# Performance work log

Hardware: AMD Instinct MI355X
Metric: run time of the kernel (lower is better)

Reference implementation:

```python
import jax, jax.numpy as jnp
import numpy as np

L = 64        # label_size = len(label2id)
START = 62    # label2id['START']
STOP = 63     # label2id['STOP']
T = 200000    # sequence length
NEG = -10000.0


def setup_inputs() -> dict:
    key = jax.random.key(0)
    k1, k2 = jax.random.split(key)
    lstm_feats = jax.random.normal(k1, (1, T, L), dtype=jnp.float32)
    transitions = jax.random.normal(k2, (L, L), dtype=jnp.float32)
    # CRF constructor masks: cannot transition INTO START, cannot transition FROM STOP
    transitions = transitions.at[START, :].set(NEG).at[:, STOP].set(NEG)
    return {"lstm_feats": lstm_feats, "transitions": transitions}


def reference(lstm_feats, transitions):
    # Viterbi decode, vectorized over tags; lax.scan over time replaces the
    # nested Python loops of the original (same recurrence, same math).
    feats = lstm_feats[0]  # (T, L)
    init = jnp.full((L,), NEG, dtype=lstm_feats.dtype).at[START].set(0.0)

    def step(v, feat):
        # scores[next, prev] = v[prev] + transitions[next, prev]
        scores = v[None, :] + transitions          # (L, L)
        bp = jnp.argmax(scores, axis=1).astype(jnp.int32)  # backpointers per next_tag
        v_new = jnp.max(scores, axis=1) + feat     # viterbi vars + emission
        return v_new, bp

    v, bptrs = jax.lax.scan(step, init, feats)     # bptrs: (T, L)

    terminal = v + transitions[STOP]               # (L,)
    best = jnp.argmax(terminal).astype(jnp.int32)
    path_score = terminal[best]

    # Backtrack: reverse scan emits the tag chosen at each time step, in order.
    def back(tag, bp):
        return bp[tag], tag

    _, best_path = jax.lax.scan(back, best, bptrs, reverse=True)  # (T,) int32
    return path_score, best_path
```

## Files before the change

kernel.cpp:

```cpp
#include <hip/hip_runtime.h>

#define L 64
#define TLEN 200000
#define CH 528
#define NCH 379
#define LASTLEN (TLEN - (NCH - 1) * CH)
#define NEGV -10000.0f
#define STARTT 62
#define STOPT 63

#define CKPT_OFF 0
#define M_OFF ((NCH + 1) * L * 4)
#define ETAG_OFF (M_OFF + NCH * L)

typedef float f32x4 __attribute__((ext_vector_type(4)));

#define WAVE_BARRIER() __asm__ volatile("s_waitcnt lgkmcnt(0)\ns_barrier" ::: "memory")
#define FAST_BARRIER() __asm__ volatile("s_barrier" ::: "memory")
#define STEP_BARRIER() __asm__ volatile("" ::: "memory")

__device__ __forceinline__ float max3f(float a, float b, float c) {
    float r;
    __asm__("v_max3_f32 %0, %1, %2, %3" : "=v"(r) : "v"(a), "v"(b), "v"(c));
    return r;
}

#define QPERM(x, ctrl)                                                         \
    __int_as_float(__builtin_amdgcn_update_dpp(                                \
        __float_as_int(x), __float_as_int(x), ctrl, 0xf, 0xf, false))

__global__ __launch_bounds__(256, 1) void k_forward(const float* __restrict__ feats,
                                                    const float* __restrict__ trans,
                                                    float* __restrict__ ckpt) {
    const int tid = threadIdx.x;
    const int l = tid & 63;
    const int w = tid >> 6;
    const int d = 16 * w + (l >> 2);
    const int g = l & 3;
    const bool writer = (g == 0);

    const f32x4* t4 = reinterpret_cast<const f32x4*>(trans) + d * 16 + g * 4;
    f32x4 q0 = t4[0], q1 = t4[1], q2 = t4[2], q3 = t4[3];
    __asm__ volatile("" : "+v"(q0), "+v"(q1), "+v"(q2), "+v"(q3));

    __shared__ __align__(16) float vbuf[2][L];

    float vq = (d == STARTT) ? 0.0f : NEGV;
    if (writer) vbuf[0][d] = vq;
    WAVE_BARRIER();

    float fc[8];
#pragma unroll
    for (int j = 0; j < 8; ++j) fc[j] = feats[j * L + d];

    int nextck = 0, cidx = 0;

#define FWD_STEP(RD, WR, FEAT)                                                 \
    do {                                                                       \
        const f32x4 va0 = *reinterpret_cast<const f32x4*>(&vbuf[RD][16 * g + 0]);  \
        const f32x4 va1 = *reinterpret_cast<const f32x4*>(&vbuf[RD][16 * g + 4]);  \
        const f32x4 va2 = *reinterpret_cast<const f32x4*>(&vbuf[RD][16 * g + 8]);  \
        const f32x4 va3 = *reinterpret_cast<const f32x4*>(&vbuf[RD][16 * g + 12]); \
        const f32x4 s0 = va0 + q0, s1 = va1 + q1, s2 = va2 + q2, s3 = va3 + q3;    \
        const float m0 = max3f(fmaxf(s0.x, s0.y), s0.z, s0.w);                 \
        const float m1 = max3f(fmaxf(s1.x, s1.y), s1.z, s1.w);                 \
        const float m2 = max3f(fmaxf(s2.x, s2.y), s2.z, s2.w);                 \
        const float m3 = max3f(fmaxf(s3.x, s3.y), s3.z, s3.w);                 \
        float x = fmaxf(max3f(m0, m1, m2), m3);                                \
        x = fmaxf(x, QPERM(x, 0xB1));                                          \
        x = fmaxf(x, QPERM(x, 0x4E));                                          \
        vq = x + (FEAT);                                                       \
        if (writer) vbuf[WR][d] = vq;                                          \
        FAST_BARRIER();                                                        \
    } while (0)

    for (int tb = 0; tb < TLEN; tb += 8) {
        if (tb == nextck) {
            if (writer) ckpt[cidx * L + d] = vq;
            nextck += CH;
            ++cidx;
        }
        float fn_[8];
        const bool more = (tb + 8) < TLEN;
        if (more) {
#pragma unroll
            for (int j = 0; j < 8; ++j) fn_[j] = feats[(tb + 8 + j) * L + d];
        }
        FWD_STEP(0, 1, fc[0]);
        FWD_STEP(1, 0, fc[1]);
        FWD_STEP(0, 1, fc[2]);
        FWD_STEP(1, 0, fc[3]);
        FWD_STEP(0, 1, fc[4]);
        FWD_STEP(1, 0, fc[5]);
        FWD_STEP(0, 1, fc[6]);
        FWD_STEP(1, 0, fc[7]);
        if (more) {
#pragma unroll
            for (int j = 0; j < 8; ++j) fc[j] = fn_[j];
        }
    }
    if (writer) ckpt[NCH * L + d] = vq;
#undef FWD_STEP
}

__device__ __forceinline__ void load_trow(const float* __restrict__ trans, int n, float* trow) {
#pragma unroll
    for (int i = 0; i < 16; ++i) {
        const f32x4 q = reinterpret_cast<const f32x4*>(trans)[n * 16 + i];
        trow[4 * i + 0] = q.x;
        trow[4 * i + 1] = q.y;
        trow[4 * i + 2] = q.z;
        trow[4 * i + 3] = q.w;
    }
}

__device__ __forceinline__ void replay_chunk(const float* __restrict__ feats,
                                             const float* __restrict__ ckpt,
                                             const float* trow, float* vsh,
                                             unsigned char* bpl, int c, int len, int n) {
    float vreg = ckpt[c * L + n];
    vsh[n] = vreg;
    STEP_BARRIER();
    const int base = c * CH;

    float fc[8];
#pragma unroll
    for (int j = 0; j < 8; ++j) fc[j] = feats[(base + j) * L + n];

    for (int sb = 0; sb < len; sb += 8) {
        float fn_[8];
        const bool more = (sb + 8) < len;
        if (more) {
#pragma unroll
            for (int j = 0; j < 8; ++j) fn_[j] = feats[(base + sb + 8 + j) * L + n];
        }
#pragma unroll
        for (int j = 0; j < 8; ++j) {
            float mc[4];
            int ic[4];
#pragma unroll
            for (int g = 0; g < 4; ++g) {
                float m = -INFINITY;
                int idx = g * 16;
#pragma unroll
                for (int r = 0; r < 4; ++r) {
                    const int pb = g * 16 + r * 4;
                    const f32x4 vv = *reinterpret_cast<const f32x4*>(vsh + pb);
                    const float a = vv.x + trow[pb + 0];
                    const float b = vv.y + trow[pb + 1];
                    const float cc = vv.z + trow[pb + 2];
                    const float d = vv.w + trow[pb + 3];
                    if (a > m)  { m = a;  idx = pb + 0; }
                    if (b > m)  { m = b;  idx = pb + 1; }
                    if (cc > m) { m = cc; idx = pb + 2; }
                    if (d > m)  { m = d;  idx = pb + 3; }
                }
                mc[g] = m;
                ic[g] = idx;
            }
            float m = mc[0];
            int idx = ic[0];
            if (mc[1] > m) { m = mc[1]; idx = ic[1]; }
            if (mc[2] > m) { m = mc[2]; idx = ic[2]; }
            if (mc[3] > m) { m = mc[3]; idx = ic[3]; }

            vreg = m + fc[j];
            bpl[(sb + j) * L + n] = (unsigned char)idx;
            vsh[n] = vreg;
            STEP_BARRIER();
        }
        if (more) {
#pragma unroll
            for (int j = 0; j < 8; ++j) fc[j] = fn_[j];
        }
    }
}

__global__ __launch_bounds__(64, 1) void k_maps(const float* __restrict__ feats,
                                                const float* __restrict__ trans,
                                                const float* __restrict__ ckpt,
                                                unsigned char* __restrict__ M) {
    const int c = blockIdx.x;
    const int n = threadIdx.x;
    const int len = (c == NCH - 1) ? LASTLEN : CH;

    __shared__ __align__(16) float vsh[L];
    __shared__ unsigned char bpl[CH * L];

    float trow[L];
    load_trow(trans, n, trow);
    replay_chunk(feats, ckpt, trow, vsh, bpl, c, len, n);
    __syncthreads();

    int tag = n;
    for (int s = len - 1; s >= 0; --s) tag = bpl[s * L + tag];
    M[c * L + n] = (unsigned char)tag;
}

__global__ __launch_bounds__(64, 1) void k_stitch(const float* __restrict__ trans,
                                                  const float* __restrict__ ckpt,
                                                  const unsigned char* __restrict__ M,
                                                  int* __restrict__ etag,
                                                  float* __restrict__ out) {
    const int n = threadIdx.x;
    __shared__ float tsh[L];
    __shared__ int bsh;
    __shared__ __align__(16) unsigned char msh[NCH * L];

    tsh[n] = ckpt[NCH * L + n] + trans[STOPT * L + n];
    __syncthreads();
    if (n == 0) {
        float m = tsh[0];
        int b = 0;
        for (int p = 1; p < L; ++p)
            if (tsh[p] > m) { m = tsh[p]; b = p; }
        out[0] = m;
        bsh = b;
    }
    __syncthreads();

    for (int i = n; i < (NCH * L) / 4; i += L)
        reinterpret_cast<int*>(msh)[i] = reinterpret_cast<const int*>(M)[i];
    __syncthreads();

    if (n == 0) {
        int carry = bsh;
        for (int c = NCH - 1; c >= 1; --c) {
            etag[c] = carry;
            carry = msh[c * L + carry];
        }
        etag[0] = carry;
    }
}

__global__ __launch_bounds__(64, 1) void k_emit(const float* __restrict__ feats,
                                                const float* __restrict__ trans,
                                                const float* __restrict__ ckpt,
                                                const int* __restrict__ etag,
                                                float* __restrict__ out) {
    const int c = blockIdx.x;
    const int n = threadIdx.x;
    const int len = (c == NCH - 1) ? LASTLEN : CH;

    __shared__ __align__(16) float vsh[L];
    __shared__ unsigned char bpl[CH * L];
    __shared__ unsigned char plc[CH];

    float trow[L];
    load_trow(trans, n, trow);
    replay_chunk(feats, ckpt, trow, vsh, bpl, c, len, n);
    __syncthreads();

    int tag = etag[c];
    for (int s = len - 1; s >= 0; --s) {
        if (n == 0) plc[s] = (unsigned char)tag;
        tag = bpl[s * L + tag];
    }
    __syncthreads();

    for (int i = n; i < len; i += L)
        out[1 + c * CH + i] = (float)plc[i];
}

extern "C" void kernel_launch(void* const* d_in, const int* in_sizes, int n_in,
                              void* d_out, int out_size, void* d_ws, size_t ws_size,
                              hipStream_t stream) {
    const float* feats = (const float*)d_in[0];
    const float* trans = (const float*)d_in[1];
    float* out = (float*)d_out;
    char* ws = (char*)d_ws;
    float* ckpt = (float*)(ws + CKPT_OFF);
    unsigned char* M = (unsigned char*)(ws + M_OFF);
    int* etag = (int*)(ws + ETAG_OFF);

    hipLaunchKernelGGL(k_forward, dim3(1), dim3(256), 0, stream, feats, trans, ckpt);
    hipLaunchKernelGGL(k_maps, dim3(NCH), dim3(64), 0, stream, feats, trans, ckpt, M);
    hipLaunchKernelGGL(k_stitch, dim3(1), dim3(64), 0, stream, trans, ckpt, M, etag, out);
    hipLaunchKernelGGL(k_emit, dim3(NCH), dim3(64), 0, stream, feats, trans, ckpt, etag, out);
}
```

Measured before the change: 35.32 ms.

## Split forward Viterbi max across waves by prev-tag range, dropping DPP reductions

The forward recurrence now gives each wave a 16-wide slice of previous tags, and each lane handles one next tag. Before, four lanes shared one next tag and combined their maxima with DPP permutes. Each wave writes a per-wave partial maximum into a 2x4x64 LDS buffer. At the start of the next step the four partials are max-combined (adding the emission to each partial is equivalent), and the checkpoints reduce the partials the same way. This removes the quad DPP reduction and the single-writer divergence from the serial step chain, but each step now issues four times as many broadcast LDS reads and three extra max ops.

```diff
diff --git a/kernel.cpp b/kernel.cpp
--- a/kernel.cpp
+++ b/kernel.cpp
@@ -25,58 +25,84 @@
     return r;
 }
 
-#define QPERM(x, ctrl)                                                         \
-    __int_as_float(__builtin_amdgcn_update_dpp(                                \
-        __float_as_int(x), __float_as_int(x), ctrl, 0xf, 0xf, false))
+__device__ __forceinline__ f32x4 vmax3q(f32x4 a, f32x4 b, f32x4 c) {
+    f32x4 r;
+    r.x = max3f(a.x, b.x, c.x);
+    r.y = max3f(a.y, b.y, c.y);
+    r.z = max3f(a.z, b.z, c.z);
+    r.w = max3f(a.w, b.w, c.w);
+    return r;
+}
+__device__ __forceinline__ f32x4 vmaxq(f32x4 a, f32x4 b) {
+    f32x4 r;
+    r.x = fmaxf(a.x, b.x);
+    r.y = fmaxf(a.y, b.y);
+    r.z = fmaxf(a.z, b.z);
+    r.w = fmaxf(a.w, b.w);
+    return r;
+}
 
 __global__ __launch_bounds__(256, 1) void k_forward(const float* __restrict__ feats,
                                                     const float* __restrict__ trans,
                                                     float* __restrict__ ckpt) {
     const int tid = threadIdx.x;
-    const int l = tid & 63;
+    const int n = tid & 63;
     const int w = tid >> 6;
-    const int d = 16 * w + (l >> 2);
-    const int g = l & 3;
-    const bool writer = (g == 0);
-
-    const f32x4* t4 = reinterpret_cast<const f32x4*>(trans) + d * 16 + g * 4;
+    const int sb = 16 * w;
+
+    const f32x4* t4 = reinterpret_cast<const f32x4*>(trans) + n * 16 + w * 4;
     f32x4 q0 = t4[0], q1 = t4[1], q2 = t4[2], q3 = t4[3];
     __asm__ volatile("" : "+v"(q0), "+v"(q1), "+v"(q2), "+v"(q3));
 
-    __shared__ __align__(16) float vbuf[2][L];
-
-    float vq = (d == STARTT) ? 0.0f : NEGV;
-    if (writer) vbuf[0][d] = vq;
+    __shared__ __align__(16) float pm[2][4][L];
+
+    pm[0][w][n] = (n == STARTT) ? 0.0f : NEGV;
     WAVE_BARRIER();
 
     float fc[8];
 #pragma unroll
-    for (int j = 0; j < 8; ++j) fc[j] = feats[j * L + d];
+    for (int j = 0; j < 8; ++j) fc[j] = feats[j * L + n];
 
     int nextck = 0, cidx = 0;
 
 #define FWD_STEP(RD, WR, FEAT)                                                 \
     do {                                                                       \
-        const f32x4 va0 = *reinterpret_cast<const f32x4*>(&vbuf[RD][16 * g + 0]);  \
-        const f32x4 va1 = *reinterpret_cast<const f32x4*>(&vbuf[RD][16 * g + 4]);  \
-        const f32x4 va2 = *reinterpret_cast<const f32x4*>(&vbuf[RD][16 * g + 8]);  \
-        const f32x4 va3 = *reinterpret_cast<const f32x4*>(&vbuf[RD][16 * g + 12]); \
-        const f32x4 s0 = va0 + q0, s1 = va1 + q1, s2 = va2 + q2, s3 = va3 + q3;    \
-        const float m0 = max3f(fmaxf(s0.x, s0.y), s0.z, s0.w);                 \
-        const float m1 = max3f(fmaxf(s1.x, s1.y), s1.z, s1.w);                 \
-        const float m2 = max3f(fmaxf(s2.x, s2.y), s2.z, s2.w);                 \
-        const float m3 = max3f(fmaxf(s3.x, s3.y), s3.z, s3.w);                 \
-        float x = fmaxf(max3f(m0, m1, m2), m3);                                \
-        x = fmaxf(x, QPERM(x, 0xB1));                                          \
-        x = fmaxf(x, QPERM(x, 0x4E));                                          \
-        vq = x + (FEAT);                                                       \
-        if (writer) vbuf[WR][d] = vq;                                          \
+        const f32x4 r0a = *reinterpret_cast<const f32x4*>(&pm[RD][0][sb + 0]); \
+        const f32x4 r1a = *reinterpret_cast<const f32x4*>(&pm[RD][1][sb + 0]); \
+        const f32x4 r2a = *reinterpret_cast<const f32x4*>(&pm[RD][2][sb + 0]); \
+        const f32x4 r3a = *reinterpret_cast<const f32x4*>(&pm[RD][3][sb + 0]); \
+        const f32x4 r0b = *reinterpret_cast<const f32x4*>(&pm[RD][0][sb + 4]); \
+        const f32x4 r1b = *reinterpret_cast<const f32x4*>(&pm[RD][1][sb + 4]); \
+        const f32x4 r2b = *reinterpret_cast<const f32x4*>(&pm[RD][2][sb + 4]); \
+        const f32x4 r3b = *reinterpret_cast<const f32x4*>(&pm[RD][3][sb + 4]); \
+        const f32x4 r0c = *reinterpret_cast<const f32x4*>(&pm[RD][0][sb + 8]); \
+        const f32x4 r1c = *reinterpret_cast<const f32x4*>(&pm[RD][1][sb + 8]); \
+        const f32x4 r2c = *reinterpret_cast<const f32x4*>(&pm[RD][2][sb + 8]); \
+        const f32x4 r3c = *reinterpret_cast<const f32x4*>(&pm[RD][3][sb + 8]); \
+        const f32x4 r0d = *reinterpret_cast<const f32x4*>(&pm[RD][0][sb + 12]);\
+        const f32x4 r1d = *reinterpret_cast<const f32x4*>(&pm[RD][1][sb + 12]);\
+        const f32x4 r2d = *reinterpret_cast<const f32x4*>(&pm[RD][2][sb + 12]);\
+        const f32x4 r3d = *reinterpret_cast<const f32x4*>(&pm[RD][3][sb + 12]);\
+        const f32x4 sa = vmaxq(vmax3q(r0a, r1a, r2a), r3a) + q0;               \
+        const f32x4 sbq = vmaxq(vmax3q(r0b, r1b, r2b), r3b) + q1;              \
+        const f32x4 sc = vmaxq(vmax3q(r0c, r1c, r2c), r3c) + q2;               \
+        const f32x4 sd = vmaxq(vmax3q(r0d, r1d, r2d), r3d) + q3;               \
+        const float m0 = max3f(fmaxf(sa.x, sa.y), sa.z, sa.w);                 \
+        const float m1 = max3f(fmaxf(sbq.x, sbq.y), sbq.z, sbq.w);             \
+        const float m2 = max3f(fmaxf(sc.x, sc.y), sc.z, sc.w);                 \
+        const float m3 = max3f(fmaxf(sd.x, sd.y), sd.z, sd.w);                 \
+        const float pmv = fmaxf(max3f(m0, m1, m2), m3) + (FEAT);               \
+        pm[WR][w][n] = pmv;                                                    \
         FAST_BARRIER();                                                        \
     } while (0)
 
     for (int tb = 0; tb < TLEN; tb += 8) {
         if (tb == nextck) {
-            if (writer) ckpt[cidx * L + d] = vq;
+            const float c0 = pm[0][0][n];
+            const float c1 = pm[0][1][n];
+            const float c2 = pm[0][2][n];
+            const float c3 = pm[0][3][n];
+            if (w == 0) ckpt[cidx * L + n] = fmaxf(max3f(c0, c1, c2), c3);
             nextck += CH;
             ++cidx;
         }
@@ -84,7 +110,7 @@
         const bool more = (tb + 8) < TLEN;
         if (more) {
 #pragma unroll
-            for (int j = 0; j < 8; ++j) fn_[j] = feats[(tb + 8 + j) * L + d];
+            for (int j = 0; j < 8; ++j) fn_[j] = feats[(tb + 8 + j) * L + n];
         }
         FWD_STEP(0, 1, fc[0]);
         FWD_STEP(1, 0, fc[1]);
@@ -99,7 +125,13 @@
             for (int j = 0; j < 8; ++j) fc[j] = fn_[j];
         }
     }
-    if (writer) ckpt[NCH * L + d] = vq;
+    {
+        const float c0 = pm[0][0][n];
+        const float c1 = pm[0][1][n];
+        const float c2 = pm[0][2][n];
+        const float c3 = pm[0][3][n];
+        if (w == 0) ckpt[NCH * L + n] = fmaxf(max3f(c0, c1, c2), c3);
+    }
 #undef FWD_STEP
 }
 
```

Result: slower. 62.83 ms (+77.9%).
